# Optimization experiments

Hardware: AMD Instinct MI355X
Metric: run time of the kernel (lower is better)

Reference implementation:

```python
import jax, jax.numpy as jnp
import numpy as np

EPS = 1e-5


def hetero_layernorm(x, node_type, gamma, beta):
    # LayerNorm over feature dim with per-node-type affine params.
    mu = jnp.mean(x, axis=-1, keepdims=True)
    var = jnp.mean(jnp.square(x - mu), axis=-1, keepdims=True)
    xn = (x - mu) * jax.lax.rsqrt(var + EPS)
    return xn * gamma[node_type] + beta[node_type]


def rgcn_conv(y, edge_src, edge_dst, edge_type, W_rel, W_root):
    # Transform per relation first (R small), then gather per-edge message.
    n = y.shape[0]
    h = jnp.einsum('nd,rde->rne', y, W_rel)          # [R, N, d]
    msg = h[edge_type, edge_src]                     # [E, d] gather
    agg = jax.ops.segment_sum(msg, edge_dst, num_segments=n)  # [N, d]
    return agg + y @ W_root


def hetero_mlp(y, node_type, W_mlp, b_mlp):
    # Per-node-type linear: compute for all T types, then select.
    n = y.shape[0]
    h = jnp.einsum('nd,tde->tne', y, W_mlp) + b_mlp[:, None, :]  # [T, N, d]
    return h[node_type, jnp.arange(n)]


def setup_inputs() -> dict:
    key = jax.random.key(0)
    ks = jax.random.split(key, 8)
    N, E, D, T, R = 50000, 800000, 128, 4, 8
    x = jax.random.normal(ks[0], (N, D), dtype=jnp.float32)
    edge_src = jax.random.randint(ks[1], (E,), 0, N, dtype=jnp.int32)
    edge_dst = jax.random.randint(ks[2], (E,), 0, N, dtype=jnp.int32)
    node_type = jax.random.randint(ks[3], (N,), 0, T, dtype=jnp.int32)
    edge_type = jax.random.randint(ks[4], (E,), 0, R, dtype=jnp.int32)
    # Scale weights ~ 1/sqrt(fan_in) for stable magnitudes.
    s = 1.0 / np.sqrt(D)
    W_rel = jax.random.normal(ks[5], (R, D, D), dtype=jnp.float32) * s
    W_root = jax.random.normal(ks[6], (D, D), dtype=jnp.float32) * s
    W_mlp = jax.random.normal(ks[7], (T, D, D), dtype=jnp.float32) * s
    return {
        'x': x, 'edge_src': edge_src, 'edge_dst': edge_dst,
        'node_type': node_type, 'edge_type': edge_type,
        'conv_gamma': jnp.ones((T, D), jnp.float32),
        'conv_beta': jnp.zeros((T, D), jnp.float32),
        'W_rel': W_rel, 'W_root': W_root,
        'mlp_gamma': jnp.ones((T, D), jnp.float32),
        'mlp_beta': jnp.zeros((T, D), jnp.float32),
        'W_mlp': W_mlp, 'b_mlp': jnp.zeros((T, D), jnp.float32),
    }


def reference(x, edge_src, edge_dst, node_type, edge_type,
              conv_gamma, conv_beta, W_rel, W_root,
              mlp_gamma, mlp_beta, W_mlp, b_mlp):
    # Norm -> Act -> (Dropout p=0, eval) -> Conv -> Residual
    y = hetero_layernorm(x, node_type, conv_gamma, conv_beta)
    y = jax.nn.relu(y)
    x = x + rgcn_conv(y, edge_src, edge_dst, edge_type, W_rel, W_root)
    # Norm -> Act -> (Dropout p=0, eval) -> MLP -> Residual
    y = hetero_layernorm(x, node_type, mlp_gamma, mlp_beta)
    y = jax.nn.relu(y)
    x = x + hetero_mlp(y, node_type, W_mlp, b_mlp)
    return x
```

## Files before the change

### kernel.cpp

```cpp
#include <hip/hip_runtime.h>
#include <hip/hip_bf16.h>

#define D 128
#define EPS 1e-5f
#define CHK 8192
#define P2CAP 6144

typedef __attribute__((ext_vector_type(8))) short short8;
typedef __attribute__((ext_vector_type(4))) float float4v;

__device__ inline ushort f2bf(float f) {
    __hip_bfloat16 b = __float2bfloat16(f);
    return *reinterpret_cast<ushort*>(&b);
}
__device__ inline float bf_lo(uint u) { return __uint_as_float(u << 16); }
__device__ inline float bf_hi(uint u) { return __uint_as_float(u & 0xffff0000u); }

__global__ void k_ln1cvt(const float* __restrict__ x, const int* __restrict__ ntp,
                         const float* __restrict__ gamma, const float* __restrict__ beta,
                         ushort* __restrict__ y,
                         const float* __restrict__ Wrel, const float* __restrict__ Wroot,
                         const float* __restrict__ Wmlp, ushort* __restrict__ Wt, int N) {
    __shared__ ushort t[128][136];
    if (blockIdx.x < 13) {
        int m = blockIdx.x;
        const float* src = (m == 0) ? Wroot
                         : (m <= 8) ? Wrel + (size_t)(m - 1) * D * D
                                    : Wmlp + (size_t)(m - 9) * D * D;
        for (int i = threadIdx.x; i < D * D; i += 256) {
            int k = i >> 7, n = i & 127;
            t[n][k] = f2bf(src[i]);
        }
        __syncthreads();
        ushort* dst = Wt + (size_t)m * D * D;
        for (int i = threadIdx.x; i < D * D; i += 256) {
            int frag = i >> 9;
            int lane = (i >> 3) & 63;
            int j = i & 7;
            int nt = frag >> 2, ks = frag & 3;
            int n = nt * 16 + (lane & 15);
            int k = ks * 32 + (lane >> 4) * 8 + j;
            dst[i] = t[n][k];
        }
        return;
    }
    int n = (blockIdx.x - 13) * 4 + (threadIdx.x >> 6);
    if (n >= N) return;
    int l = threadIdx.x & 63;
    float2 v = *(const float2*)(x + (size_t)n * D + 2 * l);
    float s = v.x + v.y, s2 = v.x * v.x + v.y * v.y;
    #pragma unroll
    for (int o = 32; o; o >>= 1) { s += __shfl_xor(s, o, 64); s2 += __shfl_xor(s2, o, 64); }
    float mu = s * (1.0f / D);
    float var = s2 * (1.0f / D) - mu * mu;
    float inv = rsqrtf(var + EPS);
    int tt = ntp[n];
    float2 g = *(const float2*)(gamma + tt * D + 2 * l);
    float2 b = *(const float2*)(beta + tt * D + 2 * l);
    float a0 = fmaxf((v.x - mu) * inv * g.x + b.x, 0.0f);
    float a1 = fmaxf((v.y - mu) * inv * g.y + b.y, 0.0f);
    ((uint*)(y + (size_t)n * D))[l] = ((uint)f2bf(a1) << 16) | f2bf(a0);
}

__global__ void k_c1(const int* __restrict__ edst, int* __restrict__ hist, int E, int B) {
    __shared__ int cnt[256];
    int c = blockIdx.x, tid = threadIdx.x;
    cnt[tid] = 0;
    __syncthreads();
    #pragma unroll 4
    for (int k = 0; k < CHK / 256; ++k) {
        int e = c * CHK + k * 256 + tid;
        if (e < E) atomicAdd(&cnt[edst[e] >> 8], 1);
    }
    __syncthreads();
    if (tid < B) hist[c * B + tid] = cnt[tid];
}
__global__ void k_c2(const int* __restrict__ hist, int* __restrict__ chunkoff,
                     int* __restrict__ bucktot, int C, int B) {
    __shared__ int v[128];
    int b = blockIdx.x, t = threadIdx.x;
    v[t] = (t < C) ? hist[t * B + b] : 0;
    __syncthreads();
    if (t == 0) {
        int s = 0;
        for (int c = 0; c < C; ++c) { int x = v[c]; v[c] = s; s += x; }
        bucktot[b] = s;
    }
    __syncthreads();
    if (t < C) chunkoff[t * B + b] = v[t];
}
__global__ void k_p1s(const int* __restrict__ edst, const int* __restrict__ esrc,
                      const int* __restrict__ etyp, const int* __restrict__ bucktot,
                      const int* __restrict__ chunkoff, uint* __restrict__ edata,
                      int E, int B) {
    __shared__ int ps[256];
    __shared__ int base[256];
    __shared__ int cnt[256];
    int c = blockIdx.x, tid = threadIdx.x;
    int bt = (tid < B) ? bucktot[tid] : 0;
    ps[tid] = bt;
    __syncthreads();
    for (int o = 1; o < 256; o <<= 1) {
        int v = (tid >= o) ? ps[tid - o] : 0;
        __syncthreads();
        ps[tid] += v;
        __syncthreads();
    }
    base[tid] = (ps[tid] - bt) + ((tid < B) ? chunkoff[c * B + tid] : 0);
    cnt[tid] = 0;
    __syncthreads();
    #pragma unroll 4
    for (int k = 0; k < CHK / 256; ++k) {
        int e = c * CHK + k * 256 + tid;
        if (e < E) {
            int d = edst[e];
            int b = d >> 8;
            int r = atomicAdd(&cnt[b], 1);
            edata[base[b] + r] =
                ((uint)esrc[e] << 12) | ((uint)(d & 255) << 4) | (uint)etyp[e];
        }
    }
}
__global__ void k_p2(const uint* __restrict__ edata, const int* __restrict__ bucktot,
                     uint* __restrict__ epack, int* __restrict__ offs,
                     int N, int E, int B) {
    __shared__ int ps[256];
    __shared__ uint ed[P2CAP];
    __shared__ int cnt[256], off[256], cur[256];
    int b = blockIdx.x, tid = threadIdx.x;
    int bt = (tid < B) ? bucktot[tid] : 0;
    ps[tid] = bt;
    __syncthreads();
    for (int o = 1; o < 256; o <<= 1) {
        int v = (tid >= o) ? ps[tid - o] : 0;
        __syncthreads();
        ps[tid] += v;
        __syncthreads();
    }
    int j0 = ps[b] - ((b < B) ? bucktot[b] : 0);
    int count = ps[b] - j0;
    if (count > P2CAP) count = P2CAP;
    for (int i = tid; i < count; i += 256) ed[i] = edata[j0 + i];
    cnt[tid] = 0;
    __syncthreads();
    for (int i = tid; i < count; i += 256) atomicAdd(&cnt[(ed[i] >> 4) & 255], 1);
    __syncthreads();
    if (tid == 0) {
        int s = 0;
        for (int i = 0; i < 256; ++i) { off[i] = s; cur[i] = s; s += cnt[i]; }
    }
    __syncthreads();
    for (int i = tid; i < count; i += 256) {
        uint v = ed[i];
        int dl = (v >> 4) & 255;
        int r = atomicAdd(&cur[dl], 1);
        epack[j0 + r] = ((v & 15u) << 28) | (v >> 12);
    }
    int v = b * 256 + tid;
    if (v < N) offs[v] = j0 + off[tid];
    if (b == 0 && tid == 0) offs[N] = E;
}

__global__ void k_zagg(const ushort* __restrict__ ybuf, const int* __restrict__ offs,
                       const uint* __restrict__ epack, ushort* __restrict__ zbuf, int N) {
    int wave = threadIdx.x >> 6;
    int l = threadIdx.x & 63;
    int v = blockIdx.x * 4 + wave;
    if (v >= N) return;
    float2 a0 = {0.f,0.f}, a1 = {0.f,0.f}, a2 = {0.f,0.f}, a3 = {0.f,0.f};
    float2 a4 = {0.f,0.f}, a5 = {0.f,0.f}, a6 = {0.f,0.f}, a7 = {0.f,0.f};
    const uint* yb = (const uint*)ybuf;
    int j = offs[v], e1 = offs[v + 1];

#define ZACC(P, U) do {                                                   \
        float lo = bf_lo(U), hi = bf_hi(U);                               \
        switch ((P) >> 28) {                                              \
            case 0: a0.x += lo; a0.y += hi; break;                        \
            case 1: a1.x += lo; a1.y += hi; break;                        \
            case 2: a2.x += lo; a2.y += hi; break;                        \
            case 3: a3.x += lo; a3.y += hi; break;                        \
            case 4: a4.x += lo; a4.y += hi; break;                        \
            case 5: a5.x += lo; a5.y += hi; break;                        \
            case 6: a6.x += lo; a6.y += hi; break;                        \
            default: a7.x += lo; a7.y += hi; break;                       \
        }                                                                 \
    } while (0)

    while (j < e1) {
        int chunk = min(64, e1 - j);
        uint pl = (j + l < e1) ? epack[j + l] : 0;
        int i = 0;
        for (; i + 3 < chunk; i += 4) {
            uint p0 = __shfl(pl, i, 64);
            uint p1 = __shfl(pl, i + 1, 64);
            uint p2 = __shfl(pl, i + 2, 64);
            uint p3 = __shfl(pl, i + 3, 64);
            uint u0 = yb[(size_t)(p0 & 0x0FFFFFFFu) * 64 + l];
            uint u1 = yb[(size_t)(p1 & 0x0FFFFFFFu) * 64 + l];
            uint u2 = yb[(size_t)(p2 & 0x0FFFFFFFu) * 64 + l];
            uint u3 = yb[(size_t)(p3 & 0x0FFFFFFFu) * 64 + l];
            ZACC(p0, u0); ZACC(p1, u1); ZACC(p2, u2); ZACC(p3, u3);
        }
        for (; i < chunk; ++i) {
            uint p = __shfl(pl, i, 64);
            uint u = yb[(size_t)(p & 0x0FFFFFFFu) * 64 + l];
            ZACC(p, u);
        }
        j += chunk;
    }
#undef ZACC
    uint* zrow = (uint*)(zbuf + (size_t)v * 1024);
    zrow[0 * 64 + l] = ((uint)f2bf(a0.y) << 16) | f2bf(a0.x);
    zrow[1 * 64 + l] = ((uint)f2bf(a1.y) << 16) | f2bf(a1.x);
    zrow[2 * 64 + l] = ((uint)f2bf(a2.y) << 16) | f2bf(a2.x);
    zrow[3 * 64 + l] = ((uint)f2bf(a3.y) << 16) | f2bf(a3.x);
    zrow[4 * 64 + l] = ((uint)f2bf(a4.y) << 16) | f2bf(a4.x);
    zrow[5 * 64 + l] = ((uint)f2bf(a5.y) << 16) | f2bf(a5.x);
    zrow[6 * 64 + l] = ((uint)f2bf(a6.y) << 16) | f2bf(a6.x);
    zrow[7 * 64 + l] = ((uint)f2bf(a7.y) << 16) | f2bf(a7.x);
}

__launch_bounds__(256)
__global__ void k_gm(const ushort* __restrict__ ybuf, const ushort* __restrict__ zbuf,
                     const ushort* __restrict__ Wt, const float* __restrict__ x,
                     const int* __restrict__ ntp,
                     const float* __restrict__ gamma, const float* __restrict__ beta,
                     const float* __restrict__ bmlp, float* __restrict__ out, int N) {
    __shared__ ushort wsm[16384];
    int tid = threadIdx.x;
    int wave = tid >> 6, lane = tid & 63;
    int quad = lane >> 4, l15 = lane & 15;
    int base = blockIdx.x * 64 + wave * 16;
    int arow = min(base + l15, N - 1);
    const ushort* yrow = ybuf + (size_t)arow * 128;
    const ushort* zrow = zbuf + (size_t)arow * 1024;

    float4v acc[8];
    #pragma unroll
    for (int nt = 0; nt < 8; ++nt) acc[nt] = (float4v){0.f, 0.f, 0.f, 0.f};

    for (int mat = 0; mat < 9; ++mat) {
        __syncthreads();
        const ushort* wsrc = Wt + (size_t)mat * 16384;
        #pragma unroll
        for (int jj = 0; jj < 8; ++jj)
            *(uint4*)(wsm + jj * 2048 + tid * 8) = *(const uint4*)(wsrc + jj * 2048 + tid * 8);
        __syncthreads();
        const ushort* ap = (mat == 0) ? yrow : zrow + (mat - 1) * 128;
        short8 a[4];
        #pragma unroll
        for (int ks = 0; ks < 4; ++ks) a[ks] = *(const short8*)(ap + ks * 32 + quad * 8);
        #pragma unroll
        for (int nt = 0; nt < 8; ++nt) {
            #pragma unroll
            for (int ks = 0; ks < 4; ++ks) {
                short8 b = *(const short8*)(wsm + (((nt * 4 + ks) * 64 + lane) << 3));
                acc[nt] = __builtin_amdgcn_mfma_f32_16x16x32_bf16(a[ks], b, acc[nt], 0, 0, 0);
            }
        }
    }

    __syncthreads();
    float s[4] = {0.f, 0.f, 0.f, 0.f}, s2[4] = {0.f, 0.f, 0.f, 0.f};
    #pragma unroll
    for (int nt = 0; nt < 8; ++nt) {
        int col = nt * 16 + l15;
        #pragma unroll
        for (int r = 0; r < 4; ++r) {
            int row = base + quad * 4 + r;
            float xv = (row < N) ? x[(size_t)row * D + col] : 0.f;
            float t = acc[nt][r] + xv;
            acc[nt][r] = t;
            s[r] += t; s2[r] += t * t;
        }
    }
    #pragma unroll
    for (int r = 0; r < 4; ++r) {
        #pragma unroll
        for (int o = 1; o < 16; o <<= 1) {
            s[r]  += __shfl_xor(s[r],  o, 64);
            s2[r] += __shfl_xor(s2[r], o, 64);
        }
    }
    int ty[4];
    #pragma unroll
    for (int r = 0; r < 4; ++r) {
        int rc = min(base + quad * 4 + r, N - 1);
        ty[r] = ntp[rc];
        float mu  = s[r] * (1.0f / D);
        float var = s2[r] * (1.0f / D) - mu * mu;
        float inv = rsqrtf(var + EPS);
        int lrow = wave * 16 + quad * 4 + r;
        #pragma unroll
        for (int nt = 0; nt < 8; ++nt) {
            int col = nt * 16 + l15;
            float yn = fmaxf((acc[nt][r] - mu) * inv * gamma[ty[r] * D + col]
                             + beta[ty[r] * D + col], 0.f);
            wsm[lrow * 136 + col] = f2bf(yn);
        }
    }
    short8 a2[4];
    const ushort* myrow = wsm + (wave * 16 + l15) * 136;
    #pragma unroll
    for (int ks = 0; ks < 4; ++ks) a2[ks] = *(const short8*)(myrow + ks * 32 + quad * 8);

    const ushort* W0 = Wt + (size_t)9  * D * D;
    const ushort* W1 = Wt + (size_t)10 * D * D;
    const ushort* W2 = Wt + (size_t)11 * D * D;
    const ushort* W3 = Wt + (size_t)12 * D * D;
    #pragma unroll
    for (int nt = 0; nt < 8; ++nt) {
        float4v c0 = {0.f,0.f,0.f,0.f}, c1 = {0.f,0.f,0.f,0.f};
        float4v c2 = {0.f,0.f,0.f,0.f}, c3 = {0.f,0.f,0.f,0.f};
        #pragma unroll
        for (int ks = 0; ks < 4; ++ks) {
            int fo = ((nt * 4 + ks) * 64 + lane) << 3;
            short8 b0 = *(const short8*)(W0 + fo);
            short8 b1 = *(const short8*)(W1 + fo);
            short8 b2 = *(const short8*)(W2 + fo);
            short8 b3 = *(const short8*)(W3 + fo);
            c0 = __builtin_amdgcn_mfma_f32_16x16x32_bf16(a2[ks], b0, c0, 0, 0, 0);
            c1 = __builtin_amdgcn_mfma_f32_16x16x32_bf16(a2[ks], b1, c1, 0, 0, 0);
            c2 = __builtin_amdgcn_mfma_f32_16x16x32_bf16(a2[ks], b2, c2, 0, 0, 0);
            c3 = __builtin_amdgcn_mfma_f32_16x16x32_bf16(a2[ks], b3, c3, 0, 0, 0);
        }
        int col = nt * 16 + l15;
        #pragma unroll
        for (int r = 0; r < 4; ++r) {
            int row = base + quad * 4 + r;
            if (row < N) {
                int t = ty[r];
                float v = (t == 0) ? c0[r] : (t == 1) ? c1[r] : (t == 2) ? c2[r] : c3[r];
                out[(size_t)row * D + col] = acc[nt][r] + v + bmlp[t * D + col];
            }
        }
    }
}

extern "C" void kernel_launch(void* const* d_in, const int* in_sizes, int n_in,
                              void* d_out, int out_size, void* d_ws, size_t ws_size,
                              hipStream_t stream) {
    const float* x          = (const float*)d_in[0];
    const int*   esrc       = (const int*)d_in[1];
    const int*   edst       = (const int*)d_in[2];
    const int*   ntyp       = (const int*)d_in[3];
    const int*   etyp       = (const int*)d_in[4];
    const float* conv_gamma = (const float*)d_in[5];
    const float* conv_beta  = (const float*)d_in[6];
    const float* W_rel      = (const float*)d_in[7];
    const float* W_root     = (const float*)d_in[8];
    const float* mlp_gamma  = (const float*)d_in[9];
    const float* mlp_beta   = (const float*)d_in[10];
    const float* W_mlp      = (const float*)d_in[11];
    const float* b_mlp      = (const float*)d_in[12];
    float* out = (float*)d_out;

    int N = in_sizes[0] / D;
    int E = in_sizes[1];
    int C = (E + CHK - 1) / CHK;
    int B = (N + 255) / 256;

    char* p = (char*)d_ws;
    auto take = [&p](size_t bytes) { char* q = p; p += (bytes + 255) & ~(size_t)255; return q; };
    ushort* ybuf    = (ushort*)take((size_t)N * D * 2);
    ushort* zbuf    = (ushort*)take((size_t)N * 1024 * 2);
    ushort* Wt      = (ushort*)take((size_t)13 * D * D * 2);
    uint*   edata   = (uint*)take((size_t)E * 4);
    uint*   epack   = (uint*)take((size_t)E * 4);
    int*    offs    = (int*)take((size_t)(N + 1) * 4);
    int*    hist    = (int*)take((size_t)C * B * 4);
    int*    chunkoff= (int*)take((size_t)C * B * 4);
    int*    bucktot = (int*)take((size_t)B * 4);

    k_ln1cvt<<<13 + (N + 3) / 4, 256, 0, stream>>>(x, ntyp, conv_gamma, conv_beta,
                                                   ybuf, W_rel, W_root, W_mlp, Wt, N);

    k_c1<<<C, 256, 0, stream>>>(edst, hist, E, B);
    k_c2<<<B, 128, 0, stream>>>(hist, chunkoff, bucktot, C, B);
    k_p1s<<<C, 256, 0, stream>>>(edst, esrc, etyp, bucktot, chunkoff, edata, E, B);
    k_p2<<<B, 256, 0, stream>>>(edata, bucktot, epack, offs, N, E, B);

    k_zagg<<<(N + 3) / 4, 256, 0, stream>>>(ybuf, offs, epack, zbuf, N);

    k_gm<<<(N + 63) / 64, 256, 0, stream>>>(ybuf, zbuf, Wt, x, ntyp,
                                            mlp_gamma, mlp_beta, b_mlp, out, N);
}
```

Before: 298.3 us.

## Give each wave two row tiles and stream B fragments from global in k_gm

k_gm now launches 128 threads per block, with each wave covering 32 rows as two 16-row MFMA groups. Each B fragment is reused across both groups. The per-matrix shared-memory staging of weights and its barriers are removed, so B operands are read straight from global memory or cache. A-fragment loads for the next matrix are double-buffered so they overlap the MFMAs of the current one. The cost is higher register pressure from two accumulator sets, and weight reads now go through L2 instead of LDS.

```diff
diff --git a/kernel.cpp b/kernel.cpp
--- a/kernel.cpp
+++ b/kernel.cpp
@@ -220,89 +220,112 @@
     zrow[7 * 64 + l] = ((uint)f2bf(a7.y) << 16) | f2bf(a7.x);
 }
 
-__launch_bounds__(256)
+__device__ __forceinline__ void aload4(short8 (&d)[2][4], const ushort* p0,
+                                       const ushort* p1, int off, int ao) {
+    #pragma unroll
+    for (int ks = 0; ks < 4; ++ks) {
+        d[0][ks] = *(const short8*)(p0 + off + ks * 32 + ao);
+        d[1][ks] = *(const short8*)(p1 + off + ks * 32 + ao);
+    }
+}
+__device__ __forceinline__ void mm2x8(float4v (&acc)[2][8], const short8 (&a)[2][4],
+                                      const ushort* __restrict__ wp, int lane) {
+    #pragma unroll
+    for (int nt = 0; nt < 8; ++nt) {
+        #pragma unroll
+        for (int ks = 0; ks < 4; ++ks) {
+            short8 b = *(const short8*)(wp + (((nt * 4 + ks) * 64 + lane) << 3));
+            acc[0][nt] = __builtin_amdgcn_mfma_f32_16x16x32_bf16(a[0][ks], b, acc[0][nt], 0, 0, 0);
+            acc[1][nt] = __builtin_amdgcn_mfma_f32_16x16x32_bf16(a[1][ks], b, acc[1][nt], 0, 0, 0);
+        }
+    }
+}
+
+__launch_bounds__(128, 2)
 __global__ void k_gm(const ushort* __restrict__ ybuf, const ushort* __restrict__ zbuf,
                      const ushort* __restrict__ Wt, const float* __restrict__ x,
                      const int* __restrict__ ntp,
                      const float* __restrict__ gamma, const float* __restrict__ beta,
                      const float* __restrict__ bmlp, float* __restrict__ out, int N) {
-    __shared__ ushort wsm[16384];
+    __shared__ ushort ysm[2][32][136];
     int tid = threadIdx.x;
     int wave = tid >> 6, lane = tid & 63;
     int quad = lane >> 4, l15 = lane & 15;
-    int base = blockIdx.x * 64 + wave * 16;
-    int arow = min(base + l15, N - 1);
-    const ushort* yrow = ybuf + (size_t)arow * 128;
-    const ushort* zrow = zbuf + (size_t)arow * 1024;
-
-    float4v acc[8];
-    #pragma unroll
-    for (int nt = 0; nt < 8; ++nt) acc[nt] = (float4v){0.f, 0.f, 0.f, 0.f};
-
-    for (int mat = 0; mat < 9; ++mat) {
-        __syncthreads();
-        const ushort* wsrc = Wt + (size_t)mat * 16384;
-        #pragma unroll
-        for (int jj = 0; jj < 8; ++jj)
-            *(uint4*)(wsm + jj * 2048 + tid * 8) = *(const uint4*)(wsrc + jj * 2048 + tid * 8);
-        __syncthreads();
-        const ushort* ap = (mat == 0) ? yrow : zrow + (mat - 1) * 128;
-        short8 a[4];
-        #pragma unroll
-        for (int ks = 0; ks < 4; ++ks) a[ks] = *(const short8*)(ap + ks * 32 + quad * 8);
-        #pragma unroll
-        for (int nt = 0; nt < 8; ++nt) {
-            #pragma unroll
-            for (int ks = 0; ks < 4; ++ks) {
-                short8 b = *(const short8*)(wsm + (((nt * 4 + ks) * 64 + lane) << 3));
-                acc[nt] = __builtin_amdgcn_mfma_f32_16x16x32_bf16(a[ks], b, acc[nt], 0, 0, 0);
-            }
-        }
-    }
-
-    __syncthreads();
-    float s[4] = {0.f, 0.f, 0.f, 0.f}, s2[4] = {0.f, 0.f, 0.f, 0.f};
-    #pragma unroll
-    for (int nt = 0; nt < 8; ++nt) {
-        int col = nt * 16 + l15;
-        #pragma unroll
-        for (int r = 0; r < 4; ++r) {
-            int row = base + quad * 4 + r;
-            float xv = (row < N) ? x[(size_t)row * D + col] : 0.f;
-            float t = acc[nt][r] + xv;
-            acc[nt][r] = t;
-            s[r] += t; s2[r] += t * t;
-        }
-    }
-    #pragma unroll
-    for (int r = 0; r < 4; ++r) {
-        #pragma unroll
-        for (int o = 1; o < 16; o <<= 1) {
-            s[r]  += __shfl_xor(s[r],  o, 64);
-            s2[r] += __shfl_xor(s2[r], o, 64);
-        }
-    }
-    int ty[4];
-    #pragma unroll
-    for (int r = 0; r < 4; ++r) {
-        int rc = min(base + quad * 4 + r, N - 1);
-        ty[r] = ntp[rc];
-        float mu  = s[r] * (1.0f / D);
-        float var = s2[r] * (1.0f / D) - mu * mu;
-        float inv = rsqrtf(var + EPS);
-        int lrow = wave * 16 + quad * 4 + r;
+    int ao = quad * 8;
+    int base = blockIdx.x * 64 + wave * 32;
+
+    const ushort* yrow0 = ybuf + (size_t)min(base + l15,      N - 1) * 128;
+    const ushort* yrow1 = ybuf + (size_t)min(base + 16 + l15, N - 1) * 128;
+    const ushort* zrow0 = zbuf + (size_t)min(base + l15,      N - 1) * 1024;
+    const ushort* zrow1 = zbuf + (size_t)min(base + 16 + l15, N - 1) * 1024;
+
+    float4v acc[2][8];
+    #pragma unroll
+    for (int g = 0; g < 2; ++g)
+        #pragma unroll
+        for (int nt = 0; nt < 8; ++nt) acc[g][nt] = (float4v){0.f, 0.f, 0.f, 0.f};
+
+    short8 aC[2][4], aN[2][4];
+    aload4(aC, yrow0, yrow1, 0, ao);
+    aload4(aN, zrow0, zrow1, 0, ao);
+    mm2x8(acc, aC, Wt, lane);
+    #pragma unroll
+    for (int mm = 0; mm < 4; ++mm) {
+        aload4(aC, zrow0, zrow1, (2 * mm + 1) * 128, ao);
+        mm2x8(acc, aN, Wt + (size_t)(2 * mm + 1) * 16384, lane);
+        if (mm < 3) aload4(aN, zrow0, zrow1, (2 * mm + 2) * 128, ao);
+        mm2x8(acc, aC, Wt + (size_t)(2 * mm + 2) * 16384, lane);
+    }
+
+    int ty[2][4];
+    #pragma unroll
+    for (int g = 0; g < 2; ++g) {
+        int gb = base + g * 16;
+        float s[4] = {0.f, 0.f, 0.f, 0.f}, s2[4] = {0.f, 0.f, 0.f, 0.f};
         #pragma unroll
         for (int nt = 0; nt < 8; ++nt) {
             int col = nt * 16 + l15;
-            float yn = fmaxf((acc[nt][r] - mu) * inv * gamma[ty[r] * D + col]
-                             + beta[ty[r] * D + col], 0.f);
-            wsm[lrow * 136 + col] = f2bf(yn);
-        }
-    }
-    short8 a2[4];
-    const ushort* myrow = wsm + (wave * 16 + l15) * 136;
-    #pragma unroll
-    for (int ks = 0; ks < 4; ++ks) a2[ks] = *(const short8*)(myrow + ks * 32 + quad * 8);
+            #pragma unroll
+            for (int r = 0; r < 4; ++r) {
+                int row = gb + quad * 4 + r;
+                float xv = (row < N) ? x[(size_t)row * D + col] : 0.f;
+                float t = acc[g][nt][r] + xv;
+                acc[g][nt][r] = t;
+                s[r] += t; s2[r] += t * t;
+            }
+        }
+        #pragma unroll
+        for (int r = 0; r < 4; ++r) {
+            #pragma unroll
+            for (int o = 1; o < 16; o <<= 1) {
+                s[r]  += __shfl_xor(s[r],  o, 64);
+                s2[r] += __shfl_xor(s2[r], o, 64);
+            }
+        }
+        #pragma unroll
+        for (int r = 0; r < 4; ++r) {
+            int rc = min(gb + quad * 4 + r, N - 1);
+            ty[g][r] = ntp[rc];
+            float mu  = s[r] * (1.0f / D);
+            float var = s2[r] * (1.0f / D) - mu * mu;
+            float inv = rsqrtf(var + EPS);
+            int lrow = g * 16 + quad * 4 + r;
+            #pragma unroll
+            for (int nt = 0; nt < 8; ++nt) {
+                int col = nt * 16 + l15;
+                float yn = fmaxf((acc[g][nt][r] - mu) * inv * gamma[ty[g][r] * D + col]
+                                 + beta[ty[g][r] * D + col], 0.f);
+                ysm[wave][lrow][col] = f2bf(yn);
+            }
+        }
+    }
+    short8 a2[2][4];
+    #pragma unroll
+    for (int g = 0; g < 2; ++g) {
+        const ushort* myrow = &ysm[wave][g * 16 + l15][0];
+        #pragma unroll
+        for (int ks = 0; ks < 4; ++ks) a2[g][ks] = *(const short8*)(myrow + ks * 32 + ao);
+    }
 
     const ushort* W0 = Wt + (size_t)9  * D * D;
     const ushort* W1 = Wt + (size_t)10 * D * D;
@@ -310,8 +333,11 @@
     const ushort* W3 = Wt + (size_t)12 * D * D;
     #pragma unroll
     for (int nt = 0; nt < 8; ++nt) {
-        float4v c0 = {0.f,0.f,0.f,0.f}, c1 = {0.f,0.f,0.f,0.f};
-        float4v c2 = {0.f,0.f,0.f,0.f}, c3 = {0.f,0.f,0.f,0.f};
+        float4v c[2][4];
+        #pragma unroll
+        for (int g = 0; g < 2; ++g)
+            #pragma unroll
+            for (int t = 0; t < 4; ++t) c[g][t] = (float4v){0.f, 0.f, 0.f, 0.f};
         #pragma unroll
         for (int ks = 0; ks < 4; ++ks) {
             int fo = ((nt * 4 + ks) * 64 + lane) << 3;
@@ -319,19 +345,26 @@
             short8 b1 = *(const short8*)(W1 + fo);
             short8 b2 = *(const short8*)(W2 + fo);
             short8 b3 = *(const short8*)(W3 + fo);
-            c0 = __builtin_amdgcn_mfma_f32_16x16x32_bf16(a2[ks], b0, c0, 0, 0, 0);
-            c1 = __builtin_amdgcn_mfma_f32_16x16x32_bf16(a2[ks], b1, c1, 0, 0, 0);
-            c2 = __builtin_amdgcn_mfma_f32_16x16x32_bf16(a2[ks], b2, c2, 0, 0, 0);
-            c3 = __builtin_amdgcn_mfma_f32_16x16x32_bf16(a2[ks], b3, c3, 0, 0, 0);
+            #pragma unroll
+            for (int g = 0; g < 2; ++g) {
+                c[g][0] = __builtin_amdgcn_mfma_f32_16x16x32_bf16(a2[g][ks], b0, c[g][0], 0, 0, 0);
+                c[g][1] = __builtin_amdgcn_mfma_f32_16x16x32_bf16(a2[g][ks], b1, c[g][1], 0, 0, 0);
+                c[g][2] = __builtin_amdgcn_mfma_f32_16x16x32_bf16(a2[g][ks], b2, c[g][2], 0, 0, 0);
+                c[g][3] = __builtin_amdgcn_mfma_f32_16x16x32_bf16(a2[g][ks], b3, c[g][3], 0, 0, 0);
+            }
         }
         int col = nt * 16 + l15;
         #pragma unroll
-        for (int r = 0; r < 4; ++r) {
-            int row = base + quad * 4 + r;
-            if (row < N) {
-                int t = ty[r];
-                float v = (t == 0) ? c0[r] : (t == 1) ? c1[r] : (t == 2) ? c2[r] : c3[r];
-                out[(size_t)row * D + col] = acc[nt][r] + v + bmlp[t * D + col];
+        for (int g = 0; g < 2; ++g) {
+            #pragma unroll
+            for (int r = 0; r < 4; ++r) {
+                int row = base + g * 16 + quad * 4 + r;
+                if (row < N) {
+                    int t = ty[g][r];
+                    float v = (t == 0) ? c[g][0][r] : (t == 1) ? c[g][1][r]
+                            : (t == 2) ? c[g][2][r] : c[g][3][r];
+                    out[(size_t)row * D + col] = acc[g][nt][r] + v + bmlp[t * D + col];
+                }
             }
         }
     }
@@ -382,6 +415,6 @@
 
     k_zagg<<<(N + 3) / 4, 256, 0, stream>>>(ybuf, offs, epack, zbuf, N);
 
-    k_gm<<<(N + 63) / 64, 256, 0, stream>>>(ybuf, zbuf, Wt, x, ntyp,
+    k_gm<<<(N + 63) / 64, 128, 0, stream>>>(ybuf, zbuf, Wt, x, ntyp,
                                             mlp_gamma, mlp_beta, b_mlp, out, N);
 }
```

After: 297.4 us. No clear change (-0.3%).

## Double-buffer weight staging in k_gm with async global-to-LDS loads

Applied to the files above, without the earlier changes.

Rewrites the fused GEMM kernel so weight matrices are staged in half-matrix chunks through double-buffered LDS using the direct global-to-LDS load builtin, overlapping each copy with MFMA work on the other buffer. The A-operand rows for the next relation are prefetched into registers while the current one computes. The MLP weights are also staged through LDS per column slice instead of being read directly from global memory. The cost is more barriers and a launch-bounds hint of two blocks per CU, which may constrain register allocation.

```diff
diff --git a/kernel.cpp b/kernel.cpp
--- a/kernel.cpp
+++ b/kernel.cpp
@@ -8,6 +8,9 @@
 
 typedef __attribute__((ext_vector_type(8))) short short8;
 typedef __attribute__((ext_vector_type(4))) float float4v;
+
+#define AS1 __attribute__((address_space(1)))
+#define AS3 __attribute__((address_space(3)))
 
 __device__ inline ushort f2bf(float f) {
     __hip_bfloat16 b = __float2bfloat16(f);
@@ -220,105 +223,146 @@
     zrow[7 * 64 + l] = ((uint)f2bf(a7.y) << 16) | f2bf(a7.x);
 }
 
-__launch_bounds__(256)
+__device__ __forceinline__ void gl_lds16(const void* g, void* l) {
+    __builtin_amdgcn_global_load_lds((const AS1 void*)g, (AS3 void*)l, 16, 0, 0);
+}
+__device__ __forceinline__ void stage_half(const ushort* __restrict__ Wt, int q,
+                                           ushort* bsm0, int wave, int lane) {
+    const char* g = (const char*)Wt + (size_t)q * 16384 + lane * 16;
+    char* l = (char*)bsm0 + (q & 1) * 16384;
+    #pragma unroll
+    for (int i = 0; i < 4; ++i) {
+        int c = i * 4 + wave;
+        gl_lds16(g + c * 1024, l + c * 1024);
+    }
+}
+__device__ __forceinline__ void stage_mlp_slice(const ushort* __restrict__ Wt, int nt,
+                                                ushort* bsm0, int wave, int lane) {
+    const char* g = (const char*)Wt + (size_t)(9 + wave) * 32768 + nt * 4096 + lane * 16;
+    char* l = (char*)bsm0 + (nt & 1) * 16384 + wave * 4096;
+    #pragma unroll
+    for (int i = 0; i < 4; ++i)
+        gl_lds16(g + i * 1024, l + i * 1024);
+}
+__device__ __forceinline__ void aloadG(short8 (&d)[4], const ushort* p, int off, int ao) {
+    #pragma unroll
+    for (int ks = 0; ks < 4; ++ks)
+        d[ks] = *(const short8*)(p + off + ks * 32 + ao);
+}
+__device__ __forceinline__ void convHalf(float4v (&acc)[8], const short8 (&a)[4],
+                                         const ushort* bsm_h, int h, int lane) {
+    #pragma unroll
+    for (int nt4 = 0; nt4 < 4; ++nt4) {
+        #pragma unroll
+        for (int ks = 0; ks < 4; ++ks) {
+            short8 b = *(const short8*)(bsm_h + (((nt4 * 4 + ks) * 64 + lane) << 3));
+            acc[h * 4 + nt4] = __builtin_amdgcn_mfma_f32_16x16x32_bf16(
+                a[ks], b, acc[h * 4 + nt4], 0, 0, 0);
+        }
+    }
+}
+
+__launch_bounds__(256, 2)
 __global__ void k_gm(const ushort* __restrict__ ybuf, const ushort* __restrict__ zbuf,
                      const ushort* __restrict__ Wt, const float* __restrict__ x,
                      const int* __restrict__ ntp,
                      const float* __restrict__ gamma, const float* __restrict__ beta,
                      const float* __restrict__ bmlp, float* __restrict__ out, int N) {
-    __shared__ ushort wsm[16384];
+    __shared__ ushort bsm[2][8192];
+    __shared__ ushort ysm[4][16][140];
+    ushort* bsm0 = &bsm[0][0];
     int tid = threadIdx.x;
     int wave = tid >> 6, lane = tid & 63;
     int quad = lane >> 4, l15 = lane & 15;
+    int ao = quad * 8;
     int base = blockIdx.x * 64 + wave * 16;
-    int arow = min(base + l15, N - 1);
-    const ushort* yrow = ybuf + (size_t)arow * 128;
-    const ushort* zrow = zbuf + (size_t)arow * 1024;
+
+    const ushort* yrow = ybuf + (size_t)min(base + l15, N - 1) * 128;
+    const ushort* zrow = zbuf + (size_t)min(base + l15, N - 1) * 1024;
 
     float4v acc[8];
     #pragma unroll
     for (int nt = 0; nt < 8; ++nt) acc[nt] = (float4v){0.f, 0.f, 0.f, 0.f};
 
-    for (int mat = 0; mat < 9; ++mat) {
-        __syncthreads();
-        const ushort* wsrc = Wt + (size_t)mat * 16384;
-        #pragma unroll
-        for (int jj = 0; jj < 8; ++jj)
-            *(uint4*)(wsm + jj * 2048 + tid * 8) = *(const uint4*)(wsrc + jj * 2048 + tid * 8);
-        __syncthreads();
-        const ushort* ap = (mat == 0) ? yrow : zrow + (mat - 1) * 128;
-        short8 a[4];
-        #pragma unroll
-        for (int ks = 0; ks < 4; ++ks) a[ks] = *(const short8*)(ap + ks * 32 + quad * 8);
-        #pragma unroll
-        for (int nt = 0; nt < 8; ++nt) {
-            #pragma unroll
-            for (int ks = 0; ks < 4; ++ks) {
-                short8 b = *(const short8*)(wsm + (((nt * 4 + ks) * 64 + lane) << 3));
-                acc[nt] = __builtin_amdgcn_mfma_f32_16x16x32_bf16(a[ks], b, acc[nt], 0, 0, 0);
-            }
-        }
-    }
-
-    __syncthreads();
-    float s[4] = {0.f, 0.f, 0.f, 0.f}, s2[4] = {0.f, 0.f, 0.f, 0.f};
-    #pragma unroll
-    for (int nt = 0; nt < 8; ++nt) {
-        int col = nt * 16 + l15;
-        #pragma unroll
-        for (int r = 0; r < 4; ++r) {
-            int row = base + quad * 4 + r;
-            float xv = (row < N) ? x[(size_t)row * D + col] : 0.f;
-            float t = acc[nt][r] + xv;
-            acc[nt][r] = t;
-            s[r] += t; s2[r] += t * t;
-        }
-    }
-    #pragma unroll
-    for (int r = 0; r < 4; ++r) {
-        #pragma unroll
-        for (int o = 1; o < 16; o <<= 1) {
-            s[r]  += __shfl_xor(s[r],  o, 64);
-            s2[r] += __shfl_xor(s2[r], o, 64);
-        }
-    }
+    short8 aC[4], aN[4];
+    stage_half(Wt, 0, bsm0, wave, lane);
+    aloadG(aC, yrow, 0, ao);
+    __syncthreads();
+
+    #pragma unroll
+    for (int m = 0; m < 9; ++m) {
+        short8 (&cur)[4] = (m & 1) ? aN : aC;
+        short8 (&nxt)[4] = (m & 1) ? aC : aN;
+        stage_half(Wt, 2 * m + 1, bsm0, wave, lane);
+        if (m < 8) aloadG(nxt, zrow, m * 128, ao);
+        convHalf(acc, cur, bsm0, 0, lane);
+        __syncthreads();
+        if (m < 8) stage_half(Wt, 2 * m + 2, bsm0, wave, lane);
+        else       stage_mlp_slice(Wt, 0, bsm0, wave, lane);
+        convHalf(acc, cur, bsm0 + 8192, 1, lane);
+        __syncthreads();
+    }
+
     int ty[4];
-    #pragma unroll
-    for (int r = 0; r < 4; ++r) {
-        int rc = min(base + quad * 4 + r, N - 1);
-        ty[r] = ntp[rc];
-        float mu  = s[r] * (1.0f / D);
-        float var = s2[r] * (1.0f / D) - mu * mu;
-        float inv = rsqrtf(var + EPS);
-        int lrow = wave * 16 + quad * 4 + r;
+    {
+        float s[4] = {0.f, 0.f, 0.f, 0.f}, s2[4] = {0.f, 0.f, 0.f, 0.f};
         #pragma unroll
         for (int nt = 0; nt < 8; ++nt) {
             int col = nt * 16 + l15;
-            float yn = fmaxf((acc[nt][r] - mu) * inv * gamma[ty[r] * D + col]
-                             + beta[ty[r] * D + col], 0.f);
-            wsm[lrow * 136 + col] = f2bf(yn);
+            #pragma unroll
+            for (int r = 0; r < 4; ++r) {
+                int row = base + quad * 4 + r;
+                float xv = (row < N) ? x[(size_t)row * D + col] : 0.f;
+                float t = acc[nt][r] + xv;
+                acc[nt][r] = t;
+                s[r] += t; s2[r] += t * t;
+            }
+        }
+        #pragma unroll
+        for (int r = 0; r < 4; ++r) {
+            #pragma unroll
+            for (int o = 1; o < 16; o <<= 1) {
+                s[r]  += __shfl_xor(s[r],  o, 64);
+                s2[r] += __shfl_xor(s2[r], o, 64);
+            }
+        }
+        #pragma unroll
+        for (int r = 0; r < 4; ++r) {
+            int rc = min(base + quad * 4 + r, N - 1);
+            ty[r] = ntp[rc];
+            float mu  = s[r] * (1.0f / D);
+            float var = s2[r] * (1.0f / D) - mu * mu;
+            float inv = rsqrtf(var + EPS);
+            int lrow = quad * 4 + r;
+            #pragma unroll
+            for (int nt = 0; nt < 8; ++nt) {
+                int col = nt * 16 + l15;
+                float yn = fmaxf((acc[nt][r] - mu) * inv * gamma[ty[r] * D + col]
+                                 + beta[ty[r] * D + col], 0.f);
+                ysm[wave][lrow][col] = f2bf(yn);
+            }
         }
     }
     short8 a2[4];
-    const ushort* myrow = wsm + (wave * 16 + l15) * 136;
-    #pragma unroll
-    for (int ks = 0; ks < 4; ++ks) a2[ks] = *(const short8*)(myrow + ks * 32 + quad * 8);
-
-    const ushort* W0 = Wt + (size_t)9  * D * D;
-    const ushort* W1 = Wt + (size_t)10 * D * D;
-    const ushort* W2 = Wt + (size_t)11 * D * D;
-    const ushort* W3 = Wt + (size_t)12 * D * D;
+    {
+        const ushort* myrow = &ysm[wave][l15][0];
+        #pragma unroll
+        for (int ks = 0; ks < 4; ++ks) a2[ks] = *(const short8*)(myrow + ks * 32 + ao);
+    }
+
     #pragma unroll
     for (int nt = 0; nt < 8; ++nt) {
+        if (nt < 7) stage_mlp_slice(Wt, nt + 1, bsm0, wave, lane);
+        const ushort* bh = bsm0 + (nt & 1) * 8192;
         float4v c0 = {0.f,0.f,0.f,0.f}, c1 = {0.f,0.f,0.f,0.f};
         float4v c2 = {0.f,0.f,0.f,0.f}, c3 = {0.f,0.f,0.f,0.f};
         #pragma unroll
         for (int ks = 0; ks < 4; ++ks) {
-            int fo = ((nt * 4 + ks) * 64 + lane) << 3;
-            short8 b0 = *(const short8*)(W0 + fo);
-            short8 b1 = *(const short8*)(W1 + fo);
-            short8 b2 = *(const short8*)(W2 + fo);
-            short8 b3 = *(const short8*)(W3 + fo);
+            int fo = (ks * 64 + lane) << 3;
+            short8 b0 = *(const short8*)(bh + 0 * 2048 + fo);
+            short8 b1 = *(const short8*)(bh + 1 * 2048 + fo);
+            short8 b2 = *(const short8*)(bh + 2 * 2048 + fo);
+            short8 b3 = *(const short8*)(bh + 3 * 2048 + fo);
             c0 = __builtin_amdgcn_mfma_f32_16x16x32_bf16(a2[ks], b0, c0, 0, 0, 0);
             c1 = __builtin_amdgcn_mfma_f32_16x16x32_bf16(a2[ks], b1, c1, 0, 0, 0);
             c2 = __builtin_amdgcn_mfma_f32_16x16x32_bf16(a2[ks], b2, c2, 0, 0, 0);
@@ -334,6 +378,7 @@
                 out[(size_t)row * D + col] = acc[nt][r] + v + bmlp[t * D + col];
             }
         }
+        if (nt < 7) __syncthreads();
     }
 }
 
```

Result: faster. 275.3 us (-7.7%).
